# Kernel optimization log

Measured on AMD Instinct MI355X. Metric: run time of the kernel, lower is better.

The kernel has to match this reference:

```python
import jax, jax.numpy as jnp
import numpy as np

B, L, U, H = 32, 2048, 512, 8
HD = U // H  # head_dim = 64


def _conv1d(x, w, b, pad):
    # x: (B, Cin, L), w: (Cout, Cin, K) -> (B, Cout, L)
    y = jax.lax.conv_general_dilated(
        x, w, window_strides=(1,), padding=[(pad, pad)],
        dimension_numbers=("NCH", "OIH", "NCH"))
    return y + b[None, :, None]


def _maxpool1d_k3(x):
    # kernel=3, stride=1, pad=1, same as nn.MaxPool1d(3,1,1)
    return jax.lax.reduce_window(
        x, -jnp.inf, jax.lax.max,
        window_dimensions=(1, 1, 3), window_strides=(1, 1, 1),
        padding=[(0, 0), (0, 0), (1, 1)])


def setup_inputs() -> dict:
    key = jax.random.key(0)
    ks = jax.random.split(key, 12)
    s = 0.02
    return {
        "t": jax.random.normal(ks[0], (B, L, U), jnp.float32),
        "g": jax.random.normal(ks[1], (B, 1, U), jnp.float32),
        "g_mask": jnp.ones((B, 1), jnp.int32),
        "t_mask": jax.random.randint(ks[2], (B, L), 0, 2).astype(jnp.int32),
        "Wq": jax.random.normal(ks[3], (U, U, 3), jnp.float32) * s,
        "bq": jnp.zeros((U,), jnp.float32),
        "Wk": jax.random.normal(ks[4], (U, U, 3), jnp.float32) * s,
        "bk": jnp.zeros((U,), jnp.float32),
        "Wv": jax.random.normal(ks[5], (U, U, 3), jnp.float32) * s,
        "bv": jnp.zeros((U,), jnp.float32),
        "Wh": jax.random.normal(ks[6], (H, H, 1), jnp.float32) * s,
        "bh": jnp.zeros((H,), jnp.float32),
        "Wo": jax.random.normal(ks[7], (U, U, 1), jnp.float32) * s,
        "bo": jnp.zeros((U,), jnp.float32),
    }


def reference(t, g, g_mask, t_mask, Wq, bq, Wk, bk, Wv, bv, Wh, bh, Wo, bo):
    x = t.transpose(0, 2, 1)                      # (B, U, L)
    q = _conv1d(x, Wq, bq, 1)                     # (B, U, L)
    k = _conv1d(x, Wk, bk, 1)
    v = _conv1d(x, Wv, bv, 1)

    # global query: max over sequence -> (B, H, 1, HD)
    q_ = q.max(-1).reshape(B, H, 1, HD)
    # keys: [global max key, maxpooled local keys] -> (B, H, 1+L, HD)
    k_g = k.max(-1).reshape(B, H, 1, HD)
    k_c = _maxpool1d_k3(k).reshape(B, H, HD, L).transpose(0, 1, 3, 2)
    key_ = jnp.concatenate([k_g, k_c], axis=2)
    v_g = v.max(-1).reshape(B, H, 1, HD)
    v_c = _maxpool1d_k3(v).reshape(B, H, HD, L).transpose(0, 1, 3, 2)
    value_ = jnp.concatenate([v_g, v_c], axis=2)

    attn = jnp.einsum("bhqd,bhkd->bhqk", q_, key_) / jnp.sqrt(jnp.float32(U))
    key_mask = jnp.concatenate([g_mask, t_mask], axis=-1)  # (B, 1+L)
    attn = jnp.where(key_mask[:, None, None, :] == 0, -jnp.inf, attn)
    attn = jax.nn.softmax(attn, axis=-1)
    # query mask multiply (g_mask broadcast over heads & keys)
    attn = attn * g_mask[:, None, :, None].astype(jnp.float32)

    out = jnp.einsum("bhqk,bhkd->bhqd", attn, value_)  # (B, H, 1, HD)
    out = out.reshape(B, H, HD)
    # conv1d_h: 1x1 conv mixing heads
    out = jnp.einsum("oi,bid->bod", Wh[:, :, 0], out) + bh[None, :, None]
    out = out.reshape(B, H, 1, HD).transpose(0, 2, 1, 3).reshape(B, 1, U)
    # conv1d_out: 1x1 conv over channels
    out = jnp.einsum("oi,bqi->bqo", Wo[:, :, 0], out) + bo
    return out  # (B, 1, U)
```

## Files before the change

kernel.cpp:

```cpp
#include <hip/hip_runtime.h>
#include <hip/hip_fp16.h>

#define B_  32
#define L_  2048
#define U_  512
#define H_  8
#define HD_ 64

typedef __attribute__((ext_vector_type(8))) _Float16 half8;
typedef __attribute__((ext_vector_type(4))) float f32x4;

struct __align__(4) H4 { __half2 lo, hi; };

__device__ __forceinline__ unsigned fmap(float x) {
    unsigned u = __float_as_uint(x);
    return (u & 0x80000000u) ? ~u : (u | 0x80000000u);
}
__device__ __forceinline__ float funmap(unsigned m) {
    unsigned bits = (m & 0x80000000u) ? (m ^ 0x80000000u) : ~m;
    return __uint_as_float(bits);
}

__global__ void __launch_bounds__(256) t_cvt(const float* __restrict__ t,
                                             __half* __restrict__ t16) {
    const size_t id = (size_t)blockIdx.x * 256 + threadIdx.x;
    const float4 a = *(const float4*)(t + id * 8);
    const float4 b = *(const float4*)(t + id * 8 + 4);
    auto p0 = __builtin_amdgcn_cvt_pkrtz(a.x, a.y);
    auto p1 = __builtin_amdgcn_cvt_pkrtz(a.z, a.w);
    auto p2 = __builtin_amdgcn_cvt_pkrtz(b.x, b.y);
    auto p3 = __builtin_amdgcn_cvt_pkrtz(b.z, b.w);
    half8 hv;
    hv[0] = p0[0]; hv[1] = p0[1]; hv[2] = p1[0]; hv[3] = p1[1];
    hv[4] = p2[0]; hv[5] = p2[1]; hv[6] = p3[0]; hv[7] = p3[1];
    *(half8*)(t16 + id * 8) = hv;
}

__global__ void __launch_bounds__(256) prep(
    const float* __restrict__ Wq, const float* __restrict__ Wk,
    const float* __restrict__ Wv, __half* __restrict__ Wrp2,
    const float* __restrict__ Wo, float* __restrict__ WoT,
    unsigned* __restrict__ maxU ) {
    const int blk = blockIdx.x;
    if (blk < 1152) {
        int id = blk * 256 + threadIdx.x;
        int mb2  = id / 12288;
        int rem  = id % 12288;
        int F    = rem >> 6;
        int lane = rem & 63;
        int mblk = mb2 >> 1, wm = mb2 & 1;
        int mi = F & 3, ks = (F >> 2) & 1, t3 = F >> 3;
        int kk = t3 % 3, iblk = t3 / 3;
        int mat = mblk >> 2;
        const float* W = (mat == 0) ? Wq : (mat == 1) ? Wk : Wv;
        int ol = ((mblk & 3) << 7) + wm * 64 + mi * 16 + (lane & 15);
        int ib = iblk * 64 + ks * 32 + (lane >> 4) * 8;
        half8 hv;
#pragma unroll
        for (int j = 0; j < 8; ++j)
            hv[j] = (_Float16)W[(ol * 512 + ib + j) * 3 + kk];
        *(half8*)(Wrp2 + (size_t)id * 8) = hv;
    } else if (blk < 2176) {
        int id = (blk - 1152) * 256 + threadIdx.x;
        int o = id & 511, i = id >> 9;
        WoT[(size_t)i * 512 + o] = Wo[(size_t)o * 512 + i];
    } else {
        int id = (blk - 2176) * 256 + threadIdx.x;
        maxU[id] = 0u; maxU[id + 16384] = 0u; maxU[id + 32768] = 0u;
    }
}

__global__ void __launch_bounds__(256, 3) conv_gemm(
    const __half* __restrict__ t16,
    const __half* __restrict__ Wrp2,
    const float* __restrict__ bq,
    const float* __restrict__ bk,
    const float* __restrict__ bv,
    __half* __restrict__ kbuf, __half* __restrict__ vbuf,
    unsigned* __restrict__ qmaxU, unsigned* __restrict__ kmaxU,
    unsigned* __restrict__ vmaxU) {
    __shared__ __align__(16) __half lB16[2][130 * 64];

    const int tid  = threadIdx.x;
    const int lane = tid & 63;
    const int w    = tid >> 6;
    const int wm = w >> 1, wn = w & 1;
    const int xcd  = blockIdx.x & 7;
    const int slot = blockIdx.x >> 3;
    const int g    = slot / 384;
    const int r    = slot % 384;
    const int chunk= r / 6;
    const int mblk = g * 6 + (r % 6);
    const int ntile= xcd + 8 * chunk;
    const int bb = ntile >> 4;
    const int l0 = (ntile & 15) << 7;
    const int lane15 = lane & 15, kgrp = lane >> 4;

    const char* Abase = (const char*)Wrp2 + (size_t)(mblk * 2 + wm) * 196608;
    const __half* tB = t16 + (size_t)bb * L_ * U_;

    f32x4 acc[4][4];
#pragma unroll
    for (int a = 0; a < 4; ++a)
#pragma unroll
        for (int c = 0; c < 4; ++c) acc[a][c] = (f32x4){0.f, 0.f, 0.f, 0.f};

    auto stageB = [&](int nb, int buf) {
        const int i0 = nb << 6;
#pragma unroll
        for (int d = 0; d < 4; ++d) {
            const int rowb = w * 32 + d * 8;
            const int row  = rowb + (lane >> 3);
            const int l    = l0 - 1 + row;
            const int p8   = lane & 7;
            const char* g2 = (const char*)(tB + (size_t)l * U_ + i0) + ((p8 ^ (l & 7)) << 4);
            if (l >= 0 && l < L_)
                __builtin_amdgcn_global_load_lds(
                    (const __attribute__((address_space(1))) unsigned int*)g2,
                    (__attribute__((address_space(3))) unsigned int*)((char*)lB16[buf] + rowb * 128),
                    16, 0, 0);
        }
        if (w == 0 && lane < 16) {
            const int row = 128 + (lane >> 3);
            const int l   = l0 - 1 + row;
            const int p8  = lane & 7;
            const char* g2 = (const char*)(tB + (size_t)l * U_ + i0) + ((p8 ^ (l & 7)) << 4);
            if (l >= 0 && l < L_)
                __builtin_amdgcn_global_load_lds(
                    (const __attribute__((address_space(1))) unsigned int*)g2,
                    (__attribute__((address_space(3))) unsigned int*)((char*)lB16[buf] + 128 * 128),
                    16, 0, 0);
        }
    };

    if (l0 == 0 && tid < 64) {
        lB16[0][tid] = (__half)0.f; lB16[1][tid] = (__half)0.f;
    }
    if (l0 == 1920 && tid < 64) {
        lB16[0][129 * 64 + tid] = (__half)0.f; lB16[1][129 * 64 + tid] = (__half)0.f;
    }

    stageB(0, 0);
    __syncthreads();

    for (int iblk = 0; iblk < 8; ++iblk) {
        const int cur = iblk & 1;
        const char* bbase = (const char*)lB16[cur];
#pragma unroll
        for (int kk = 0; kk < 3; ++kk) {
#pragma unroll
            for (int ks = 0; ks < 2; ++ks) {
                half8 af[4];
#pragma unroll
                for (int mi = 0; mi < 4; ++mi)
                    af[mi] = *(const half8*)(Abase +
                        ((((size_t)iblk * 3 + kk) * 2 + ks) * 4 + mi) * 1024 + lane * 16);
                if (kk == 0 && ks == 0 && iblk < 7) stageB(iblk + 1, cur ^ 1);
                half8 bfr[4];
#pragma unroll
                for (int ni = 0; ni < 4; ++ni) {
                    const int rbuf = wn * 64 + ni * 16 + lane15 + kk;
                    const int key  = (rbuf + 7) & 7;
                    const int p    = ks * 4 + kgrp;
                    bfr[ni] = *(const half8*)(bbase + rbuf * 128 + ((p ^ key) << 4));
                }
#pragma unroll
                for (int mi = 0; mi < 4; ++mi)
#pragma unroll
                    for (int ni = 0; ni < 4; ++ni)
                        acc[mi][ni] = __builtin_amdgcn_mfma_f32_16x16x32_f16(
                            af[mi], bfr[ni], acc[mi][ni], 0, 0, 0);
            }
        }
        __syncthreads();
    }

    const int mat = mblk >> 2;
    const float* bias = (mat == 0) ? bq : (mat == 1) ? bk : bv;
    const int oBase = ((mblk & 3) << 7) + wm * 64 + kgrp * 4;
#pragma unroll
    for (int mi = 0; mi < 4; ++mi) {
#pragma unroll
        for (int r2 = 0; r2 < 4; ++r2) {
            const int o = oBase + mi * 16 + r2;
            const float bsv = bias[o];
            float vals[4];
            float mx = -3.0e38f;
#pragma unroll
            for (int ni = 0; ni < 4; ++ni) {
                float v = acc[mi][ni][r2] + bsv;
                vals[ni] = v;
                mx = fmaxf(mx, v);
            }
#pragma unroll
            for (int d = 1; d < 16; d <<= 1) mx = fmaxf(mx, __shfl_xor(mx, d, 64));
            if (mat == 0) {
                if (lane15 == 0) atomicMax(&qmaxU[bb * U_ + o], fmap(mx));
            } else {
                __half* buf = (mat == 1) ? kbuf : vbuf;
                size_t rowbase = ((size_t)bb * U_ + o) * L_ + l0 + wn * 64;
#pragma unroll
                for (int ni = 0; ni < 4; ++ni)
                    buf[rowbase + ni * 16 + lane15] = __float2half(vals[ni]);
                unsigned* mptr = (mat == 1) ? kmaxU : vmaxU;
                if (lane15 == 0) atomicMax(&mptr[bb * U_ + o], fmap(mx));
            }
        }
    }
}

__global__ void __launch_bounds__(1024) attn_kernel(
    const __half* __restrict__ kbuf, const __half* __restrict__ vbuf,
    const unsigned* __restrict__ qmaxU, const unsigned* __restrict__ kmaxU,
    const unsigned* __restrict__ vmaxU,
    const int* __restrict__ g_mask, const int* __restrict__ t_mask,
    float* __restrict__ attout) {
    const int bh = blockIdx.x;
    const int b = bh >> 3, h = bh & 7;
    const int tid = threadIdx.x;
    const int lane = tid & 63;
    const int wid = tid >> 6;
    __shared__ float qs[64], kg[64], vg[64];
    __shared__ float pl[2048];
    __shared__ float wredA[16], wredB[16];
    if (tid < 64) {
        qs[tid] = funmap(qmaxU[b * U_ + h * 64 + tid]);
        kg[tid] = funmap(kmaxU[b * U_ + h * 64 + tid]);
        vg[tid] = funmap(vmaxU[b * U_ + h * 64 + tid]);
    }
    __syncthreads();
    const float scale = 0.044194173824159216f;

    const __half* kbase = kbuf + ((size_t)b * U_ + h * 64) * L_;
    const int l0 = tid * 2;
    const bool mE = (l0 == 0), pE = (l0 + 2 >= L_);
    const int offm2 = mE ? 0 : l0 - 2;
    const int offp  = pE ? L_ - 2 : l0 + 2;
    float acc0 = 0.f, acc1 = 0.f;
    {
        const __half* pr = kbase;
#pragma unroll 4
        for (int o = 0; o < 64; ++o) {
            const H4 w4 = *(const H4*)(pr + offm2);
            const __half2 hp = *(const __half2*)(pr + offp);
            const float f1 = mE ? __half2float(w4.lo.x) : __half2float(w4.hi.x);
            const float f2 = mE ? __half2float(w4.lo.y) : __half2float(w4.hi.y);
            const float fL = mE ? -3.0e38f : __half2float(w4.lo.y);
            const float fR = pE ? -3.0e38f : __half2float(hp.x);
            const float qw = qs[o];
            acc0 += qw * fmaxf(fL, fmaxf(f1, f2));
            acc1 += qw * fmaxf(f1, fmaxf(f2, fR));
            pr += L_;
        }
    }
    float lg0, lg1;
    {
        const int tm0 = t_mask[b * L_ + l0], tm1 = t_mask[b * L_ + l0 + 1];
        lg0 = (tm0 == 0) ? -INFINITY : acc0 * scale;
        lg1 = (tm1 == 0) ? -INFINITY : acc1 * scale;
    }
    float lmax = fmaxf(lg0, lg1);
#pragma unroll
    for (int d = 1; d < 64; d <<= 1) lmax = fmaxf(lmax, __shfl_xor(lmax, d, 64));
    if (lane == 0) wredA[wid] = lmax;
    float ag = 0.f;
#pragma unroll 8
    for (int d = 0; d < 64; ++d) ag += qs[d] * kg[d];
    const int gm = g_mask[b];
    const float lgg = gm ? ag * scale : -INFINITY;
    __syncthreads();
    float mx = lgg;
#pragma unroll
    for (int i = 0; i < 16; ++i) mx = fmaxf(mx, wredA[i]);
    const float e0 = (lg0 <= -3.0e38f) ? 0.f : __expf(lg0 - mx);
    const float e1 = (lg1 <= -3.0e38f) ? 0.f : __expf(lg1 - mx);
    pl[l0] = e0; pl[l0 + 1] = e1;
    float psum = e0 + e1;
#pragma unroll
    for (int d = 1; d < 64; d <<= 1) psum += __shfl_xor(psum, d, 64);
    if (lane == 0) wredB[wid] = psum;
    __syncthreads();
    const float eg = gm ? __expf(lgg - mx) : 0.f;
    float den = eg;
#pragma unroll
    for (int i = 0; i < 16; ++i) den += wredB[i];
    if (!(den > 0.f)) den = 1.f;
    const int o = tid >> 4;
    const int ch = tid & 15;
    const __half* vrow = vbuf + ((size_t)b * U_ + h * 64 + o) * L_;
    float s = 0.f;
#pragma unroll 2
    for (int it = 0; it < 16; ++it) {
        const int lb = it * 128 + ch * 8;
        union { uint4 u; __half hh[8]; } pk;
        pk.u = *(const uint4*)(vrow + lb);
        float f[10];
#pragma unroll
        for (int j = 0; j < 8; ++j) f[j + 1] = __half2float(pk.hh[j]);
        f[0] = (lb == 0) ? -3.0e38f : __half2float(vrow[lb - 1]);
        f[9] = (lb + 8 >= L_) ? -3.0e38f : __half2float(vrow[lb + 8]);
#pragma unroll
        for (int j = 0; j < 8; ++j)
            s += pl[lb + j] * fmaxf(f[j], fmaxf(f[j + 1], f[j + 2]));
    }
#pragma unroll
    for (int d = 1; d < 16; d <<= 1) s += __shfl_xor(s, d, 64);
    if (ch == 0) {
        float val = (eg * vg[o] + s) / den;
        val *= (float)gm;
        attout[(size_t)b * U_ + h * 64 + o] = val;
    }
}

__global__ void __launch_bounds__(512) out_kernel(
    const float* __restrict__ attout,
    const float* __restrict__ Wh, const float* __restrict__ bh,
    const float* __restrict__ WoT, const float* __restrict__ bo,
    float* __restrict__ out) {
    const int b  = blockIdx.x >> 3;
    const int chk = blockIdx.x & 7;
    const int tid = threadIdx.x;
    __shared__ float tmp[512];
    __shared__ float part[8][64];
    {
        const int oh = tid >> 6, d = tid & 63;
        float s = bh[oh];
#pragma unroll
        for (int i = 0; i < 8; ++i)
            s += Wh[oh * 8 + i] * attout[b * U_ + i * 64 + d];
        tmp[oh * 64 + d] = s;
    }
    __syncthreads();
    const int p  = tid >> 6;
    const int ol = tid & 63;
    const int o  = chk * 64 + ol;
    float s2 = 0.f;
#pragma unroll 8
    for (int i = p * 64; i < p * 64 + 64; ++i)
        s2 += WoT[(size_t)i * 512 + o] * tmp[i];
    part[p][ol] = s2;
    __syncthreads();
    if (tid < 64) {
        float tot = bo[chk * 64 + tid];
#pragma unroll
        for (int q = 0; q < 8; ++q) tot += part[q][tid];
        out[b * U_ + chk * 64 + tid] = tot;
    }
}

extern "C" void kernel_launch(void* const* d_in, const int* in_sizes, int n_in,
                              void* d_out, int out_size, void* d_ws, size_t ws_size,
                              hipStream_t stream) {
    const float* t  = (const float*)d_in[0];
    const int* g_mask = (const int*)d_in[2];
    const int* t_mask = (const int*)d_in[3];
    const float* Wq = (const float*)d_in[4];
    const float* bq = (const float*)d_in[5];
    const float* Wk = (const float*)d_in[6];
    const float* bk = (const float*)d_in[7];
    const float* Wv = (const float*)d_in[8];
    const float* bv = (const float*)d_in[9];
    const float* Wh = (const float*)d_in[10];
    const float* bh = (const float*)d_in[11];
    const float* Wo = (const float*)d_in[12];
    const float* bo = (const float*)d_in[13];

    char* ws = (char*)d_ws;
    __half* Wrp2 = (__half*)ws;
    float* WoT   = (float*)(ws + 4718592);
    __half* t16  = (__half*)(ws + 5767168);
    __half* kbuf = (__half*)(ws + 5767168 + 67108864);
    __half* vbuf = (__half*)(ws + 5767168 + 2 * 67108864);
    unsigned* qmaxU = (unsigned*)(ws + 5767168 + 3 * 67108864);
    unsigned* kmaxU = qmaxU + 16384;
    unsigned* vmaxU = kmaxU + 16384;
    float* attout = (float*)(vmaxU + 16384);

    prep<<<2240, 256, 0, stream>>>(Wq, Wk, Wv, Wrp2, Wo, WoT, qmaxU);
    t_cvt<<<16384, 256, 0, stream>>>(t, t16);
    conv_gemm<<<6144, 256, 0, stream>>>(t16, Wrp2, bq, bk, bv, kbuf, vbuf,
                                        qmaxU, kmaxU, vmaxU);
    attn_kernel<<<256, 1024, 0, stream>>>(kbuf, vbuf, qmaxU, kmaxU, vmaxU,
                                          g_mask, t_mask, attout);
    out_kernel<<<256, 512, 0, stream>>>(attout, Wh, bh, WoT, bo, (float*)d_out);
}
```

Baseline: 595.7 us.

## Split attention into key-logit and value passes with global atomic max

```diff
diff --git a/kernel.cpp b/kernel.cpp
--- a/kernel.cpp
+++ b/kernel.cpp
@@ -23,24 +23,28 @@
 
 __global__ void __launch_bounds__(256) t_cvt(const float* __restrict__ t,
                                              __half* __restrict__ t16) {
-    const size_t id = (size_t)blockIdx.x * 256 + threadIdx.x;
-    const float4 a = *(const float4*)(t + id * 8);
-    const float4 b = *(const float4*)(t + id * 8 + 4);
-    auto p0 = __builtin_amdgcn_cvt_pkrtz(a.x, a.y);
-    auto p1 = __builtin_amdgcn_cvt_pkrtz(a.z, a.w);
-    auto p2 = __builtin_amdgcn_cvt_pkrtz(b.x, b.y);
-    auto p3 = __builtin_amdgcn_cvt_pkrtz(b.z, b.w);
-    half8 hv;
-    hv[0] = p0[0]; hv[1] = p0[1]; hv[2] = p1[0]; hv[3] = p1[1];
-    hv[4] = p2[0]; hv[5] = p2[1]; hv[6] = p3[0]; hv[7] = p3[1];
-    *(half8*)(t16 + id * 8) = hv;
+    const size_t total = (size_t)B_ * L_ * U_ / 8;
+    for (size_t id = (size_t)blockIdx.x * 256 + threadIdx.x; id < total;
+         id += (size_t)2048 * 256) {
+        const float4 a = *(const float4*)(t + id * 8);
+        const float4 b = *(const float4*)(t + id * 8 + 4);
+        auto p0 = __builtin_amdgcn_cvt_pkrtz(a.x, a.y);
+        auto p1 = __builtin_amdgcn_cvt_pkrtz(a.z, a.w);
+        auto p2 = __builtin_amdgcn_cvt_pkrtz(b.x, b.y);
+        auto p3 = __builtin_amdgcn_cvt_pkrtz(b.z, b.w);
+        half8 hv;
+        hv[0] = p0[0]; hv[1] = p0[1]; hv[2] = p1[0]; hv[3] = p1[1];
+        hv[4] = p2[0]; hv[5] = p2[1]; hv[6] = p3[0]; hv[7] = p3[1];
+        *(half8*)(t16 + id * 8) = hv;
+    }
 }
 
 __global__ void __launch_bounds__(256) prep(
     const float* __restrict__ Wq, const float* __restrict__ Wk,
     const float* __restrict__ Wv, __half* __restrict__ Wrp2,
     const float* __restrict__ Wo, float* __restrict__ WoT,
-    unsigned* __restrict__ maxU ) {
+    unsigned* __restrict__ maxU ,
+    unsigned* __restrict__ bhmax) {
     const int blk = blockIdx.x;
     if (blk < 1152) {
         int id = blk * 256 + threadIdx.x;
@@ -67,6 +71,8 @@
     } else {
         int id = (blk - 2176) * 256 + threadIdx.x;
         maxU[id] = 0u; maxU[id + 16384] = 0u; maxU[id + 32768] = 0u;
+        if (blk == 2176 && threadIdx.x < 256)
+            bhmax[threadIdx.x] = fmap(-3.0e38f);
     }
 }
 
@@ -209,30 +215,22 @@
     }
 }
 
-__global__ void __launch_bounds__(1024) attn_kernel(
-    const __half* __restrict__ kbuf, const __half* __restrict__ vbuf,
-    const unsigned* __restrict__ qmaxU, const unsigned* __restrict__ kmaxU,
-    const unsigned* __restrict__ vmaxU,
-    const int* __restrict__ g_mask, const int* __restrict__ t_mask,
-    float* __restrict__ attout) {
-    const int bh = blockIdx.x;
+__global__ void __launch_bounds__(512) attn_k(
+    const __half* __restrict__ kbuf, const unsigned* __restrict__ qmaxU,
+    const int* __restrict__ t_mask,
+    float* __restrict__ plraw, unsigned* __restrict__ bhmax) {
+    const int bh = blockIdx.x >> 1;
+    const int lc = blockIdx.x & 1;
     const int b = bh >> 3, h = bh & 7;
     const int tid = threadIdx.x;
     const int lane = tid & 63;
-    const int wid = tid >> 6;
-    __shared__ float qs[64], kg[64], vg[64];
-    __shared__ float pl[2048];
-    __shared__ float wredA[16], wredB[16];
-    if (tid < 64) {
-        qs[tid] = funmap(qmaxU[b * U_ + h * 64 + tid]);
-        kg[tid] = funmap(kmaxU[b * U_ + h * 64 + tid]);
-        vg[tid] = funmap(vmaxU[b * U_ + h * 64 + tid]);
-    }
+    __shared__ float qs[64];
+    if (tid < 64) qs[tid] = funmap(qmaxU[b * U_ + h * 64 + tid]);
     __syncthreads();
     const float scale = 0.044194173824159216f;
 
     const __half* kbase = kbuf + ((size_t)b * U_ + h * 64) * L_;
-    const int l0 = tid * 2;
+    const int l0 = lc * 1024 + tid * 2;
     const bool mE = (l0 == 0), pE = (l0 + 2 >= L_);
     const int offm2 = mE ? 0 : l0 - 2;
     const int offp  = pE ? L_ - 2 : l0 + 2;
@@ -253,27 +251,48 @@
             pr += L_;
         }
     }
-    float lg0, lg1;
-    {
-        const int tm0 = t_mask[b * L_ + l0], tm1 = t_mask[b * L_ + l0 + 1];
-        lg0 = (tm0 == 0) ? -INFINITY : acc0 * scale;
-        lg1 = (tm1 == 0) ? -INFINITY : acc1 * scale;
-    }
+    const int tm0 = t_mask[b * L_ + l0], tm1 = t_mask[b * L_ + l0 + 1];
+    const float lg0 = (tm0 == 0) ? -INFINITY : acc0 * scale;
+    const float lg1 = (tm1 == 0) ? -INFINITY : acc1 * scale;
+    *(float2*)(plraw + (size_t)bh * L_ + l0) = make_float2(lg0, lg1);
     float lmax = fmaxf(lg0, lg1);
 #pragma unroll
     for (int d = 1; d < 64; d <<= 1) lmax = fmaxf(lmax, __shfl_xor(lmax, d, 64));
-    if (lane == 0) wredA[wid] = lmax;
+    if (lane == 0) atomicMax(&bhmax[bh], fmap(lmax));
+}
+
+__global__ void __launch_bounds__(1024) attn_v(
+    const __half* __restrict__ vbuf,
+    const unsigned* __restrict__ qmaxU, const unsigned* __restrict__ kmaxU,
+    const unsigned* __restrict__ vmaxU, const unsigned* __restrict__ bhmax,
+    const float* __restrict__ plraw,
+    const int* __restrict__ g_mask, float* __restrict__ attout) {
+    const int bh = blockIdx.x;
+    const int b = bh >> 3, h = bh & 7;
+    const int tid = threadIdx.x;
+    const int lane = tid & 63;
+    const int wid = tid >> 6;
+    __shared__ float qs[64], kg[64], vg[64];
+    __shared__ float pl[2048];
+    __shared__ float wredB[16];
+    if (tid < 64) {
+        qs[tid] = funmap(qmaxU[b * U_ + h * 64 + tid]);
+        kg[tid] = funmap(kmaxU[b * U_ + h * 64 + tid]);
+        vg[tid] = funmap(vmaxU[b * U_ + h * 64 + tid]);
+    }
+    __syncthreads();
+    const float scale = 0.044194173824159216f;
+
+    const int l0 = tid * 2;
+    const float2 lg = *(const float2*)(plraw + (size_t)bh * L_ + l0);
     float ag = 0.f;
 #pragma unroll 8
     for (int d = 0; d < 64; ++d) ag += qs[d] * kg[d];
     const int gm = g_mask[b];
     const float lgg = gm ? ag * scale : -INFINITY;
-    __syncthreads();
-    float mx = lgg;
-#pragma unroll
-    for (int i = 0; i < 16; ++i) mx = fmaxf(mx, wredA[i]);
-    const float e0 = (lg0 <= -3.0e38f) ? 0.f : __expf(lg0 - mx);
-    const float e1 = (lg1 <= -3.0e38f) ? 0.f : __expf(lg1 - mx);
+    const float mx = fmaxf(funmap(bhmax[bh]), lgg);
+    const float e0 = (lg.x <= -3.0e38f) ? 0.f : __expf(lg.x - mx);
+    const float e1 = (lg.y <= -3.0e38f) ? 0.f : __expf(lg.y - mx);
     pl[l0] = e0; pl[l0 + 1] = e1;
     float psum = e0 + e1;
 #pragma unroll
@@ -375,12 +394,15 @@
     unsigned* kmaxU = qmaxU + 16384;
     unsigned* vmaxU = kmaxU + 16384;
     float* attout = (float*)(vmaxU + 16384);
-
-    prep<<<2240, 256, 0, stream>>>(Wq, Wk, Wv, Wrp2, Wo, WoT, qmaxU);
-    t_cvt<<<16384, 256, 0, stream>>>(t, t16);
+    unsigned* bhmax = (unsigned*)(attout + 16384);
+    float* plraw = (float*)t16;
+
+    prep<<<2240, 256, 0, stream>>>(Wq, Wk, Wv, Wrp2, Wo, WoT, qmaxU, bhmax);
+    t_cvt<<<2048, 256, 0, stream>>>(t, t16);
     conv_gemm<<<6144, 256, 0, stream>>>(t16, Wrp2, bq, bk, bv, kbuf, vbuf,
                                         qmaxU, kmaxU, vmaxU);
-    attn_kernel<<<256, 1024, 0, stream>>>(kbuf, vbuf, qmaxU, kmaxU, vmaxU,
-                                          g_mask, t_mask, attout);
+    attn_k<<<512, 512, 0, stream>>>(kbuf, qmaxU, t_mask, plraw, bhmax);
+    attn_v<<<256, 1024, 0, stream>>>(vbuf, qmaxU, kmaxU, vmaxU, bhmax, plraw,
+                                     g_mask, attout);
     out_kernel<<<256, 512, 0, stream>>>(attout, Wh, bh, WoT, bo, (float*)d_out);
 }
```

After: 607.4 us. No clear change (+2.0%).
